# Kernel tuning notes

Measured on AMD Instinct MI355X. Metric: run time of the kernel, lower is better.

## Reference

```python
import jax, jax.numpy as jnp
import numpy as np

V, FN, CIN, HID, PTS = 50000, 100000, 3, 256, 10000
TEMP = 0.1
EPS = 1e-20


def line_mesh_graph(f, Vn):
    # f: [F,3] int triangles. Build the 'line mesh': one node per unique mesh edge.
    fe = jnp.concatenate([f[:, :2], f[:, 1:], f[:, jnp.array([2, 0])]], 0)  # [3F,2]
    fe = jnp.sort(fe, axis=1)
    keys = fe[:, 0] * Vn + fe[:, 1]                       # [3F] unique key per undirected edge
    ukeys, inv = jnp.unique(keys, return_inverse=True)
    edge_node = jnp.stack([ukeys // Vn, ukeys % Vn], -1)  # [E,2] endpoints of each edge-node
    E = ukeys.shape[0]
    feid = inv.reshape(3, -1).T                           # [F,3] edge-node id per face edge
    # line-graph connectivity: edges of the same face are mutual neighbors, plus self-loops
    srcs, dsts = [], []
    for i, j in ((0, 1), (1, 0), (1, 2), (2, 1), (2, 0), (0, 2)):
        srcs.append(feid[:, i]); dsts.append(feid[:, j])
    loop = jnp.arange(E)
    edge = jnp.stack([jnp.concatenate(srcs + [loop]), jnp.concatenate(dsts + [loop])], 0)  # [2,NE]
    return edge, edge_node, keys


def gsn_conv(x, edge, Ws, Wn, b):
    # GSNConv stand-in: self transform + mean-aggregated neighbor transform
    s, d = edge[0], edge[1]
    N = x.shape[0]
    deg = jax.ops.segment_sum(jnp.ones_like(s, x.dtype), d, num_segments=N)
    agg = jax.ops.segment_sum(x[s], d, num_segments=N) / jnp.clip(deg, 1.0)[:, None]
    return x @ Ws + agg @ Wn + b


def gumbel_mask(logits, temperature, num, key):
    U = jax.random.uniform(key, logits.shape)
    g = -jnp.log(-jnp.log(U + EPS) + EPS)
    y = jax.nn.softmax((logits + g) / temperature, -1)[:, 0]  # [E]
    _, ind = jax.lax.top_k(y, num)
    y_hard = jnp.zeros_like(y).at[ind].set(1.0)
    mask = jax.lax.stop_gradient(y_hard - y) + y              # straight-through one-hot
    return mask, y_hard == 1.0


def mesh_collapse(f, keys, pool_edge, Vn):
    # Vectorized replacement of the per-pool-edge python loop: hash-join pooled edge keys
    # against all 3F face-edge keys via sorted search.
    PE = pool_edge.shape[0]
    pool_idx = jnp.arange(Vn, Vn + PE)
    edge_keys = keys.reshape(3, -1).T                     # [F,3] (cols: e01,e12,e20)
    pk = pool_edge[:, 0] * Vn + pool_edge[:, 1]
    order = jnp.argsort(pk); pks = pk[order]
    flat = edge_keys.reshape(-1)
    pos = jnp.clip(jnp.searchsorted(pks, flat), 0, PE - 1)
    found = pks[pos] == flat
    pei = jnp.where(found, pool_idx[order[pos]], -1).reshape(-1, 3)  # pool_edge_idx [F,3]
    fm = found.reshape(-1, 3)
    pen = fm.sum(1)                                       # pool_edge_num per face
    psi = (fm * jnp.arange(3)).sum(1)                     # pool_start_idx per face
    vv = jnp.stack([f[:, 0], pei[:, 0], f[:, 1], pei[:, 1], f[:, 2], pei[:, 2]], -1)
    nf0 = f[pen == 0]
    fv1 = vv[pen == 1]; s1 = psi[pen == 1]
    fv1 = jnp.concatenate([fv1[s1 == 0], jnp.roll(fv1[s1 == 1], -2, 1), jnp.roll(fv1[s1 == 2], 2, 1)], 0)
    nf1 = jnp.concatenate([jnp.stack([fv1[:, 0], fv1[:, 1], fv1[:, 4]], -1),
                           jnp.stack([fv1[:, 1], fv1[:, 2], fv1[:, 4]], -1)], 0)
    fv2 = vv[pen == 2]; s2 = psi[pen == 2]
    fv2 = jnp.concatenate([fv2[s2 == 1], jnp.roll(fv2[s2 == 2], 2, 1), jnp.roll(fv2[s2 == 3], -2, 1)], 0)
    nf2 = jnp.concatenate([jnp.stack([fv2[:, 0], fv2[:, 1], fv2[:, 4]], -1),
                           jnp.stack([fv2[:, 1], fv2[:, 2], fv2[:, 3]], -1),
                           jnp.stack([fv2[:, 1], fv2[:, 3], fv2[:, 4]], -1)], 0)
    fv3 = vv[pen == 3]
    nf3 = jnp.concatenate([jnp.stack([fv3[:, 0], fv3[:, 1], fv3[:, 5]], -1),
                           jnp.stack([fv3[:, 1], fv3[:, 2], fv3[:, 3]], -1),
                           jnp.stack([fv3[:, 1], fv3[:, 3], fv3[:, 5]], -1),
                           jnp.stack([fv3[:, 3], fv3[:, 4], fv3[:, 5]], -1)], 0)
    new_faces = jnp.concatenate([nf0, nf1, nf2, nf3], 0)
    ne = jnp.concatenate([new_faces[:, :2], new_faces[:, 1:], new_faces[:, jnp.array([2, 0])]], 0)
    ai = jnp.arange(Vn + PE)
    ne = jnp.concatenate([jnp.stack([ai, ai], -1), ne], 0)
    return new_faces, ne.T


def setup_inputs():
    key = jax.random.key(0)
    ks = jax.random.split(key, 10)
    s1 = 1.0 / np.sqrt(CIN); s2 = 1.0 / np.sqrt(HID)
    return {
        'input': jax.random.normal(ks[0], (1, V, CIN), jnp.float32),
        'face': jax.random.randint(ks[1], (1, FN, 3), 0, V),
        'coord': jax.random.normal(ks[2], (1, V, 3), jnp.float32),
        'detail_points': jax.random.normal(ks[3], (1, PTS, 3), jnp.float32),
        'div': 5,
        'W1s': jax.random.normal(ks[4], (CIN, HID), jnp.float32) * s1,
        'W1n': jax.random.normal(ks[5], (CIN, HID), jnp.float32) * s1,
        'b1': jnp.zeros((HID,), jnp.float32),
        'W2s': jax.random.normal(ks[6], (HID, 2), jnp.float32) * s2,
        'W2n': jax.random.normal(ks[7], (HID, 2), jnp.float32) * s2,
        'b2': jnp.zeros((2,), jnp.float32),
    }


def reference(input, face, coord, detail_points, div, W1s, W1n, b1, W2s, W2n, b2):
    # B=1 (data-dependent per-sample output sizes make batch stacking only valid then)
    x0, f = input[0], face[0]
    Vn = x0.shape[0]
    edge, edge_node, keys = line_mesh_graph(f, Vn)
    xe = 0.5 * (x0[edge_node[:, 0]] + x0[edge_node[:, 1]])   # edge-node features [E,C]
    h = jax.nn.relu(gsn_conv(xe, edge, W1s, W1n, b1))
    out = jax.nn.sigmoid(gsn_conv(h, edge, W2s, W2n, b2))    # [E,2]
    mask, pool_ind = gumbel_mask(out, TEMP, out.shape[0] // div, jax.random.key(42))
    pool_edge = edge_node[pool_ind]                          # [PE,2]
    new_faces, new_edges = mesh_collapse(f, keys, pool_edge, Vn)
    return edge_node[None], new_faces[None], new_edges[None], mask[None]
```

## Files before the change

kernel.cpp:

```cpp
#include <hip/hip_runtime.h>
#include <stdint.h>

typedef uint32_t u32;
typedef uint64_t u64;

#define VN 50000
#define FN 100000
#define K3F 300000
#define EMAX 300000
#define NB1 1172
#define NBS 293
#define NBH 293
#define NBC 98
#define HALF1 150016
#define NBL 586

#define W_KPA    0u
#define W_KPB    600000u
#define W_SEGOFF 1200000u
#define W_FEID   1500004u
#define W_XE     1800004u
#define W_PK     2700004u
#define W_P      2703076u
#define W_Q      3303076u
#define W_Y      3903076u
#define W_YMAP   4203076u
#define W_T64    4503076u
#define W_SEL    5103140u
#define W_SELR   5403140u
#define W_CAT    5703140u
#define W_CATR   5803140u
#define W_NFI    5903140u
#define W_HIST   7103140u
#define W_HIST2  7403172u
#define W_SUMS   7703204u
#define W_CATH   7707300u
#define W_TKH    7708324u
#define W_DONE   7708580u
#define W_SCAL   7708612u

#define S_E 0
#define S_NUM 1
#define S_PFX 2
#define S_KREM 3
#define S_TU 4
#define S_R 5
#define S_NF 6
#define S_NEN 7
#define S_O1 8
#define S_O2 9
#define S_O3 10
#define S_RS 16
#define S_GS 24
#define S_GP 32

__device__ __forceinline__ void tf2x32(u32 x0, u32 x1, u32& o0, u32& o1) {
  const u32 ks0 = 0u, ks1 = 42u, ks2 = 0x1BD11BDAu ^ 0u ^ 42u;
  x0 += ks0; x1 += ks1;
#define TFR(r) { x0 += x1; x1 = (x1<<(r))|(x1>>(32-(r))); x1 ^= x0; }
  TFR(13) TFR(15) TFR(26) TFR(6)   x0 += ks1; x1 += ks2 + 1u;
  TFR(17) TFR(29) TFR(16) TFR(24)  x0 += ks2; x1 += ks0 + 2u;
  TFR(13) TFR(15) TFR(26) TFR(6)   x0 += ks0; x1 += ks1 + 3u;
  TFR(17) TFR(29) TFR(16) TFR(24)  x0 += ks1; x1 += ks2 + 4u;
  TFR(13) TFR(15) TFR(26) TFR(6)   x0 += ks2; x1 += ks0 + 5u;
#undef TFR
  o0 = x0; o1 = x1;
}

__global__ void scan_blocks(const u32* __restrict__ in, u32* __restrict__ out,
                            u32* __restrict__ sums, int n, u32* __restrict__ zeronext) {
  __shared__ u32 lds[256];
  int t = threadIdx.x;
  int base = blockIdx.x*1024 + t*4;
  u32 v[4]; u32 tot = 0;
  for (int k = 0; k < 4; ++k) { v[k] = (base+k < n) ? in[base+k] : 0u; tot += v[k]; }
  lds[t] = tot; __syncthreads();
  for (int o = 1; o < 256; o <<= 1) {
    u32 x = (t >= o) ? lds[t-o] : 0u; __syncthreads();
    lds[t] += x; __syncthreads();
  }
  u32 excl = lds[t] - tot;
  if (t == 255) sums[blockIdx.x] = lds[255];
  u32 run = excl;
  for (int k = 0; k < 4; ++k) {
    if (base+k < n) {
      out[base+k] = run;
      if (zeronext) zeronext[base+k] = 0u;
    }
    run += v[k];
  }
}

__global__ void scan_flagblocks(const u64* __restrict__ kp, u32* __restrict__ out,
                                u32* __restrict__ sums, int n) {
  __shared__ u32 lds[256];
  int t = threadIdx.x;
  int base = blockIdx.x*1024 + t*4;
  u32 v[4]; u32 tot = 0;
  for (int k = 0; k < 4; ++k) {
    int i = base + k;
    u32 f = 0;
    if (i < n) f = (i == 0 || (u32)(kp[i-1]>>32) != (u32)(kp[i]>>32)) ? 1u : 0u;
    v[k] = f; tot += f;
  }
  lds[t] = tot; __syncthreads();
  for (int o = 1; o < 256; o <<= 1) {
    u32 x = (t >= o) ? lds[t-o] : 0u; __syncthreads();
    lds[t] += x; __syncthreads();
  }
  u32 excl = lds[t] - tot;
  if (t == 255) sums[blockIdx.x] = lds[255];
  u32 run = excl;
  for (int k = 0; k < 4; ++k) { if (base+k < n) out[base+k] = run; run += v[k]; }
}

__global__ void scan_sums(u32* __restrict__ s, int nb) {
  __shared__ u32 lds[256];
  __shared__ u32 carry;
  int t = threadIdx.x;
  if (t == 0) carry = 0;
  __syncthreads();
  for (int base = 0; base < nb; base += 1024) {
    int idx = base + t*4;
    u32 v[4]; u32 tot = 0;
    for (int k = 0; k < 4; ++k) { v[k] = (idx+k < nb) ? s[idx+k] : 0u; tot += v[k]; }
    lds[t] = tot; __syncthreads();
    for (int o = 1; o < 256; o <<= 1) {
      u32 x = (t >= o) ? lds[t-o] : 0u; __syncthreads();
      lds[t] += x; __syncthreads();
    }
    u32 excl = lds[t] - tot;
    u32 ctot = lds[255];
    u32 c = carry;
    __syncthreads();
    u32 run = c + excl;
    for (int k = 0; k < 4; ++k) { if (idx+k < nb) s[idx+k] = run; run += v[k]; }
    if (t == 0) carry = c + ctot;
    __syncthreads();
  }
}

__global__ void scan64_src(const u32* __restrict__ ymap, const u32* __restrict__ scal,
                           u64* __restrict__ part, u64* __restrict__ sums) {
  __shared__ u64 lds[256];
  int t = threadIdx.x;
  int base = blockIdx.x*1024 + t*4;
  int E = (int)scal[S_E];
  u32 TU = scal[S_TU];
  u64 v[4]; u64 tot = 0;
  for (int k = 0; k < 4; ++k) {
    int e = base + k;
    u64 val = 0;
    if (e < E) {
      u32 u = ymap[e];
      if (u > TU) val = 1ull;
      else if (u == TU) val = 1ull << 32;
    }
    v[k] = val; tot += val;
  }
  lds[t] = tot; __syncthreads();
  for (int o = 1; o < 256; o <<= 1) {
    u64 x = (t >= o) ? lds[t-o] : 0ull; __syncthreads();
    lds[t] += x; __syncthreads();
  }
  u64 excl = lds[t] - tot;
  if (t == 255) sums[blockIdx.x] = lds[255];
  u64 run = excl;
  for (int k = 0; k < 4; ++k) { part[base+k] = run; run += v[k]; }
}

__global__ void scan64_sums(u64* __restrict__ s, int nb) {
  __shared__ u64 lds[256];
  int t = threadIdx.x;
  int idx = t*4;
  u64 v[4]; u64 tot = 0;
  for (int k = 0; k < 4; ++k) { v[k] = (idx+k < nb) ? s[idx+k] : 0ull; tot += v[k]; }
  lds[t] = tot; __syncthreads();
  for (int o = 1; o < 256; o <<= 1) {
    u64 x = (t >= o) ? lds[t-o] : 0ull; __syncthreads();
    lds[t] += x; __syncthreads();
  }
  u64 excl = lds[t] - tot;
  u64 run = excl;
  for (int k = 0; k < 4; ++k) { if (idx+k < nb) s[idx+k] = run; run += v[k]; }
}

__global__ void k_sel2(const u32* __restrict__ ymap, const u64* __restrict__ part,
                       const u64* __restrict__ sums, const u32* __restrict__ scal,
                       u32* __restrict__ sel, u32* __restrict__ selr) {
  int e = blockIdx.x*256 + threadIdx.x;
  if (e >= EMAX) return;
  int E = (int)scal[S_E];
  u32 TU = scal[S_TU], R = scal[S_R];
  u64 pre = part[e] + sums[e>>10];
  u32 GTpre = (u32)pre, TIEpre = (u32)(pre >> 32);
  u32 v = 0;
  if (e < E) {
    u32 u = ymap[e];
    v = (u > TU) || (u == TU && TIEpre < R);
  }
  sel[e] = v ? 1u : 0u;
  selr[e] = GTpre + min(TIEpre, R);
}

__global__ void k_rscat(const u64* __restrict__ kp, u64* __restrict__ okp,
                        const u32* __restrict__ hist, const u32* __restrict__ sums,
                        int shift, int nb, u32* __restrict__ histnext) {
  __shared__ u64 ball[4][8];
  __shared__ u64 vmask[4];
  int t = threadIdx.x, w = t>>6, lane = t&63;
  int i = blockIdx.x*256 + t;
  bool valid = i < K3F;
  u64 v = valid ? kp[i] : 0ull;
  u32 d = ((u32)(v>>32) >> shift) & 255u;
  for (int bit = 0; bit < 8; ++bit) {
    u64 bm = __ballot(valid && ((d>>bit)&1u));
    if (lane == 0) ball[w][bit] = bm;
  }
  u64 vb = __ballot(valid ? 1 : 0);
  if (lane == 0) vmask[w] = vb;
  __syncthreads();
  if (valid) {
    u32 rank = 0;
    for (int ww = 0; ww < w; ++ww) {
      u64 m = vmask[ww];
      for (int bit = 0; bit < 8; ++bit) { u64 bb = ball[ww][bit]; m &= ((d>>bit)&1u) ? bb : ~bb; }
      rank += (u32)__popcll(m);
    }
    u64 m = vmask[w];
    for (int bit = 0; bit < 8; ++bit) { u64 bb = ball[w][bit]; m &= ((d>>bit)&1u) ? bb : ~bb; }
    rank += (u32)__popcll(m & ((1ull<<lane)-1ull));
    u32 h = d*(u32)nb + blockIdx.x;
    u32 pos = hist[h] + sums[h>>10] + rank;
    okp[pos] = v;
    if (histnext) {
      u32 d2 = ((u32)(v>>32) >> (shift+8)) & 255u;
      atomicAdd(&histnext[d2*(u32)nb + (pos>>8)], 1u);
    }
  }
}

__global__ void k_keys(const int* __restrict__ face,
                       const float* __restrict__ W1s, const float* __restrict__ W1n,
                       const float* __restrict__ b1,
                       const float* __restrict__ W2s, const float* __restrict__ W2n,
                       float* __restrict__ pk,
                       u64* __restrict__ kp, u32* __restrict__ hist,
                       u32* __restrict__ tkh, u32* __restrict__ done) {
  __shared__ u32 h[256];
  int t = threadIdx.x;
  h[t] = 0;
  __syncthreads();
  if (blockIdx.x == 0) {
    tkh[t] = 0u;
    if (t < 32) done[t] = 0u;
    float* p = pk + t*12;
    p[0] = W1s[t]; p[1] = W1s[256+t]; p[2] = W1s[512+t];
    p[3] = W1n[t]; p[4] = W1n[256+t]; p[5] = W1n[512+t];
    p[6] = b1[t];
    p[7] = W2s[2*t]; p[8] = W2s[2*t+1];
    p[9] = W2n[2*t]; p[10] = W2n[2*t+1];
    p[11] = 0.0f;
  }
  int i = blockIdx.x*256 + t;
  if (i < K3F) {
    int s = i / FN, f = i - s*FN;
    int v0 = face[f*3 + s];
    int v1 = face[f*3 + (s == 2 ? 0 : s+1)];
    int a = min(v0, v1), b = max(v0, v1);
    u32 key = ((u32)a * (u32)VN + (u32)b) ^ 0x80000000u;
    kp[i] = ((u64)key << 32) | (u32)i;
    atomicAdd(&h[key & 255u], 1u);
  }
  __syncthreads();
  hist[(u32)t*NB1 + blockIdx.x] = h[t];
}

__global__ void k_uwrite(const u64* __restrict__ kp, const u32* __restrict__ rankp,
                         const u32* __restrict__ sums, const float* __restrict__ x,
                         u32* __restrict__ segoff, u32* __restrict__ feid,
                         float* __restrict__ xe, float* __restrict__ dout,
                         u32* __restrict__ scal, const int* __restrict__ divp) {
  int p = blockIdx.x*256 + threadIdx.x;
  if (p >= K3F) return;
  u64 v = kp[p];
  u32 cur = (u32)(v >> 32);
  u32 fl = (p == 0 || (u32)(kp[p-1] >> 32) != cur) ? 1u : 0u;
  u32 rk = rankp[p] + sums[p>>10];
  if (fl) {
    u32 e = rk;
    segoff[e] = (u32)p;
    int k = (int)(cur ^ 0x80000000u);
    long long kk = (long long)k;
    long long qq = (kk - (kk < 0 ? (long long)(VN-1) : 0ll)) / VN;
    int q = (int)qq;
    int r = (int)(kk - qq * VN);
    dout[2*e]   = (float)q;
    dout[2*e+1] = (float)r;
    u32 i0 = (u32)(q < 0 ? q + VN : q);
    u32 i1 = (u32)r;
    for (int c = 0; c < 3; ++c) xe[e*3+c] = 0.5f*(x[i0*3+c] + x[i1*3+c]);
  }
  u32 id = rk - 1u + fl;
  u32 i = (u32)v;
  u32 s = i / FN, f = i - s*FN;
  feid[f*3 + s] = id;
  if (p == K3F-1) {
    u32 E = rk + fl;
    u32 num = E / (u32)divp[0];
    scal[S_E] = E; scal[S_NUM] = num;
    segoff[E] = (u32)K3F;
    scal[S_PFX] = 0u; scal[S_KREM] = num;
  }
}

__device__ __forceinline__ void agg_neighbors(int e, u32 st, u32 en,
                                              const u64* __restrict__ kp,
                                              const u32* __restrict__ feid,
                                              const float* __restrict__ v, int stride,
                                              float* acc0, float* acc1, float* acc2) {
  const int sslot[6] = {0,1,1,2,2,0};
  const int dslot[6] = {1,0,2,1,0,2};
  float c0 = 0.f, c1 = 0.f, c2 = 0.f;
  for (int b = 0; b < 6; ++b) {
    int j = dslot[b], isl = sslot[b];
    for (u32 p = st; p < en; ++p) {
      u32 i = (u32)kp[p];
      u32 s = i / FN;
      if ((int)s == j) {
        u32 f = i - s*FN;
        u32 u = feid[f*3 + isl];
        c0 += v[u*stride]; c1 += v[u*stride+1]; if (stride == 3) c2 += v[u*stride+2];
      }
    }
  }
  c0 += v[e*stride]; c1 += v[e*stride+1]; if (stride == 3) c2 += v[e*stride+2];
  *acc0 = c0; *acc1 = c1; *acc2 = c2;
}

__global__ void k_l12(const float* __restrict__ xe, const u32* __restrict__ segoff,
                      const u64* __restrict__ kp, const u32* __restrict__ feid,
                      const u32* __restrict__ scal, const float* __restrict__ pk,
                      float* __restrict__ P, float* __restrict__ Q) {
  int e1 = blockIdx.x*256 + threadIdx.x;
  int E = (int)scal[S_E];
  if (e1 >= E) return;
  int e2 = e1 + HALF1;
  bool v2 = e2 < E;
  int e2c = v2 ? e2 : e1;
  u32 st1 = segoff[e1], en1 = segoff[e1+1];
  u32 st2 = segoff[e2c], en2 = segoff[e2c+1];
  float c0a,c1a,c2a, c0b,c1b,c2b;
  agg_neighbors(e1,  st1, en1, kp, feid, xe, 3, &c0a,&c1a,&c2a);
  agg_neighbors(e2c, st2, en2, kp, feid, xe, 3, &c0b,&c1b,&c2b);
  float x0a=xe[e1*3],  x1a=xe[e1*3+1],  x2a=xe[e1*3+2];
  float x0b=xe[e2c*3], x1b=xe[e2c*3+1], x2b=xe[e2c*3+2];
  float dga = (float)(2u*(en1-st1)+1u), dgb = (float)(2u*(en2-st2)+1u);
  float m0a=c0a/dga, m1a=c1a/dga, m2a=c2a/dga;
  float m0b=c0b/dgb, m1b=c1b/dgb, m2b=c2b/dgb;
  float p0a=0,p1a=0,q0a=0,q1a=0, p0b=0,p1b=0,q0b=0,q1b=0;
#pragma unroll 4
  for (int hh = 0; hh < 256; ++hh) {
    const float* w = pk + hh*12;
    float w0=w[0],w1=w[1],w2=w[2],w3=w[3],w4=w[4],w5=w[5],w6=w[6];
    float w7=w[7],w8=w[8],w9=w[9],w10=w[10];
    float s1a = x0a*w0 + x1a*w1 + x2a*w2;
    float s2a = m0a*w3 + m1a*w4 + m2a*w5;
    float ha = fmaxf(s1a + s2a + w6, 0.0f);
    p0a += ha*w7;  p1a += ha*w8;  q0a += ha*w9;  q1a += ha*w10;
    float s1b = x0b*w0 + x1b*w1 + x2b*w2;
    float s2b = m0b*w3 + m1b*w4 + m2b*w5;
    float hb = fmaxf(s1b + s2b + w6, 0.0f);
    p0b += hb*w7;  p1b += hb*w8;  q0b += hb*w9;  q1b += hb*w10;
  }
  P[2*e1] = p0a; P[2*e1+1] = p1a; Q[2*e1] = q0a; Q[2*e1+1] = q1a;
  if (v2) { P[2*e2] = p0b; P[2*e2+1] = p1b; Q[2*e2] = q0b; Q[2*e2+1] = q1b; }
}

__device__ __forceinline__ void score_one(int e, const float* P, const float* Q,
                                          const u32* segoff, const u64* kp, const u32* feid,
                                          float b20, float b21, float* yo, u32* ymo) {
  u32 st = segoff[e], en = segoff[e+1];
  float a0, a1, dummy;
  agg_neighbors(e, st, en, kp, feid, Q, 2, &a0, &a1, &dummy);
  float dg = (float)(2u*(en - st) + 1u);
  float z0 = P[2*e]   + a0/dg + b20;
  float z1 = P[2*e+1] + a1/dg + b21;
  float l0 = 1.0f/(1.0f + expf(-z0));
  float l1 = 1.0f/(1.0f + expf(-z1));
  u32 g0b, g1b;
  { u32 o0,o1; tf2x32(0u, 2u*(u32)e,      o0, o1); g0b = o0 ^ o1; }
  { u32 o0,o1; tf2x32(0u, 2u*(u32)e + 1u, o0, o1); g1b = o0 ^ o1; }
  float U0 = __uint_as_float((g0b>>9) | 0x3f800000u) - 1.0f;
  float U1 = __uint_as_float((g1b>>9) | 0x3f800000u) - 1.0f;
  float g0 = -logf(-logf(U0 + 1e-20f) + 1e-20f);
  float g1 = -logf(-logf(U1 + 1e-20f) + 1e-20f);
  float A0 = (l0 + g0)/0.1f;
  float A1 = (l1 + g1)/0.1f;
  float mx = fmaxf(A0, A1);
  float e0 = expf(A0-mx), e1v = expf(A1-mx);
  float y = e0/(e0+e1v);
  *yo = y;
  *ymo = __float_as_uint(y) | 0x80000000u;
}

__global__ void k_scores(const float* __restrict__ P, const float* __restrict__ Q,
                         const u32* __restrict__ segoff, const u64* __restrict__ kp,
                         const u32* __restrict__ feid,
                         const float* __restrict__ b2, const u32* __restrict__ scal,
                         float* __restrict__ Y, u32* __restrict__ ymap) {
  int e1 = blockIdx.x*256 + threadIdx.x;
  int E = (int)scal[S_E];
  if (e1 >= E) return;
  int e2 = e1 + HALF1;
  bool v2 = e2 < E;
  int e2c = v2 ? e2 : e1;
  float b20 = b2[0], b21 = b2[1];
  float ya, yb; u32 ma, mb;
  score_one(e1,  P, Q, segoff, kp, feid, b20, b21, &ya, &ma);
  score_one(e2c, P, Q, segoff, kp, feid, b20, b21, &yb, &mb);
  Y[e1] = ya; ymap[e1] = ma;
  if (v2) { Y[e2] = yb; ymap[e2] = mb; }
}

__global__ void k_tkround(const u32* __restrict__ ymap, u32* __restrict__ scal,
                          u32* __restrict__ hist, u32* __restrict__ done, int byte) {
  __shared__ u32 h[256];
  __shared__ u32 s2[256];
  __shared__ u32 chosen_s;
  __shared__ u32 lastflag;
  int t = threadIdx.x;
  h[t] = 0u;
  if (t == 0) lastflag = 0u;
  __syncthreads();
  int E = (int)scal[S_E];
  u32 pfx = scal[S_PFX];
  int base = blockIdx.x*1024;
  for (int k = 0; k < 4; ++k) {
    int e = base + k*256 + t;
    if (e < E) {
      u32 u = ymap[e];
      bool match = (byte == 3) || ((u >> ((byte+1)*8)) == pfx);
      if (match) atomicAdd(&h[(u >> (byte*8)) & 255u], 1u);
    }
  }
  __syncthreads();
  u32 c = h[t];
  if (c) atomicAdd(&hist[t], c);
  __syncthreads();
  if (t == 0) {
    __threadfence();
    u32 old = atomicAdd(&done[byte], 1u);
    if (old == gridDim.x - 1u) lastflag = 1u;
  }
  __syncthreads();
  if (!lastflag) return;
  __threadfence();
  u32 v = atomicExch(&hist[t], 0u);
  s2[t] = v;
  if (t == 0) chosen_s = 0u;
  __syncthreads();
  for (int o = 1; o < 256; o <<= 1) {
    u32 x = (t + o < 256) ? s2[t+o] : 0u; __syncthreads();
    s2[t] += x; __syncthreads();
  }
  u32 krem = scal[S_KREM];
  if (s2[t] >= krem) atomicMax(&chosen_s, (u32)t);
  __syncthreads();
  if (t == 0) {
    u32 chosen = chosen_s;
    u32 sufnext = (chosen < 255u) ? s2[chosen+1] : 0u;
    u32 newkrem = krem - sufnext;
    u32 npfx = (scal[S_PFX] << 8) | chosen;
    scal[S_PFX] = npfx; scal[S_KREM] = newkrem;
    if (byte == 0) { scal[S_TU] = npfx; scal[S_R] = newkrem; }
  }
}

__global__ void k_catfused(const u32* __restrict__ feid, const u32* __restrict__ sel,
                           u32* __restrict__ cat, u32* __restrict__ ch) {
  __shared__ u32 h[8];
  int t = threadIdx.x;
  if (t < 8) h[t] = 0u;
  __syncthreads();
  int base = blockIdx.x*1024 + t*4;
  for (int k = 0; k < 4; ++k) {
    int f = base + k;
    if (f < FN) {
      u32 m0 = sel[feid[f*3]], m1 = sel[feid[f*3+1]], m2 = sel[feid[f*3+2]];
      u32 pen = m0 + m1 + m2;
      u32 psi = m1 + 2u*m2;
      u32 c = (pen == 0) ? 0u : (pen == 1) ? (1u+psi) : (pen == 2) ? (3u+psi) : 7u;
      cat[f] = c;
      atomicAdd(&h[c], 1u);
    }
  }
  __syncthreads();
  if (t < 8) ch[(u32)t*NBC + blockIdx.x] = h[t];
}

__global__ void k_catoff(u32* __restrict__ ch, u32* __restrict__ scal) {
  __shared__ u32 lds[256];
  __shared__ u32 ex[1024];
  int t = threadIdx.x;
  u32 v[4]; u32 tot = 0;
  for (int k = 0; k < 4; ++k) {
    int i = t*4 + k;
    u32 x = (i < 8*NBC) ? ch[i] : 0u;
    v[k] = x; tot += x;
  }
  lds[t] = tot; __syncthreads();
  for (int o = 1; o < 256; o <<= 1) {
    u32 x = (t >= o) ? lds[t-o] : 0u; __syncthreads();
    lds[t] += x; __syncthreads();
  }
  u32 excl = lds[t] - tot;
  u32 run = excl;
  for (int k = 0; k < 4; ++k) { ex[t*4+k] = run; run += v[k]; }
  __syncthreads();
  for (int k = 0; k < 4; ++k) {
    int i = t*4 + k;
    if (i < 8*NBC) ch[i] = ex[i];
  }
  if (t == 0) {
    u32 total = lds[255];
    u32 bnd[9];
    for (int c = 0; c < 8; ++c) bnd[c] = ex[c*NBC];
    bnd[8] = total;
    u32 tot8[8];
    for (int c = 0; c < 8; ++c) tot8[c] = bnd[c+1] - bnd[c];
    u32 n0 = tot8[0], n1 = tot8[1]+tot8[2]+tot8[3], n2 = tot8[4]+tot8[5]+tot8[6], n3 = tot8[7];
    u32 NF = n0 + 2u*n1 + 3u*n2 + 4u*n3;
    u32 E = scal[S_E], num = scal[S_NUM];
    u32 NEn = (u32)VN + num + 3u*NF;
    scal[S_NF] = NF; scal[S_NEN] = NEn;
    scal[S_O1] = 2u*E;
    scal[S_O2] = 2u*E + 3u*NF;
    scal[S_O3] = 2u*E + 3u*NF + 2u*NEn;
    u32 RS[8] = {0u, n0,n0,n0, n0+2u*n1, n0+2u*n1, n0+2u*n1, n0+2u*n1+3u*n2};
    u32 GS[8] = {0u, n1,n1,n1, n2,n2,n2, n3};
    u32 GP[8] = {0u, n0,n0,n0, n0+n1, n0+n1, n0+n1, n0+n1+n2};
    for (int i = 0; i < 8; ++i) { scal[S_RS+i] = RS[i]; scal[S_GS+i] = GS[i]; scal[S_GP+i] = GP[i]; }
  }
}

__global__ void k_catrank(const u32* __restrict__ cat, const u32* __restrict__ ch,
                          u32* __restrict__ cr) {
  __shared__ u32 lds[256];
  int t = threadIdx.x;
  int base = blockIdx.x*1024 + t*4;
  u32 cc[4], loc[4];
  u32 cnt[8] = {0,0,0,0,0,0,0,0};
  for (int k = 0; k < 4; ++k) {
    int i = base + k;
    if (i < FN) { u32 c = cat[i]; cc[k] = c; loc[k] = cnt[c]++; }
    else cc[k] = 8u;
  }
  u32 tb[8];
  for (int c = 0; c < 8; ++c) {
    lds[t] = cnt[c]; __syncthreads();
    for (int o = 1; o < 256; o <<= 1) {
      u32 x = (t >= o) ? lds[t-o] : 0u; __syncthreads();
      lds[t] += x; __syncthreads();
    }
    tb[c] = lds[t] - cnt[c];
    __syncthreads();
  }
  for (int k = 0; k < 4; ++k) {
    int i = base + k;
    if (i < FN) { u32 c = cc[k]; cr[i] = ch[c*NBC + blockIdx.x] + tb[c] + loc[k]; }
  }
}

__global__ void k_wfaces(const int* __restrict__ face, const u32* __restrict__ cat,
                         const u32* __restrict__ cr, const u32* __restrict__ feid,
                         const u32* __restrict__ selr, const u32* __restrict__ scal,
                         int* __restrict__ nfi, float* __restrict__ dout) {
  int f = blockIdx.x*256 + threadIdx.x;
  if (f >= FN) return;
  const int nfc[8] = {1,2,2,2,3,3,3,4};
  const int tri[8][4][3] = {
    {{0,2,4},{0,0,0},{0,0,0},{0,0,0}},
    {{0,1,4},{1,2,4},{0,0,0},{0,0,0}},
    {{2,3,0},{3,4,0},{0,0,0},{0,0,0}},
    {{4,5,2},{5,0,2},{0,0,0},{0,0,0}},
    {{0,1,4},{1,2,3},{1,3,4},{0,0,0}},
    {{4,5,2},{5,0,1},{5,1,2},{0,0,0}},
    {{2,3,0},{3,4,5},{3,5,0},{0,0,0}},
    {{0,1,5},{1,2,3},{1,3,5},{3,4,5}}};
  u32 c = cat[f];
  int cv[6];
  cv[0] = face[f*3];   cv[2] = face[f*3+1]; cv[4] = face[f*3+2];
  cv[1] = VN + (int)selr[feid[f*3]];
  cv[3] = VN + (int)selr[feid[f*3+1]];
  cv[5] = VN + (int)selr[feid[f*3+2]];
  u32 g  = cr[f] - scal[S_GP + c];
  u32 o1 = scal[S_O1];
  for (int j = 0; j < nfc[c]; ++j) {
    u32 row = scal[S_RS + c] + (u32)j*scal[S_GS + c] + g;
    for (int m = 0; m < 3; ++m) {
      int v = cv[tri[c][j][m]];
      nfi[row*3 + m] = v;
      dout[o1 + row*3 + m] = (float)v;
    }
  }
}

__global__ void k_wne(const int* __restrict__ nfi, const u32* __restrict__ scal,
                      float* __restrict__ dout) {
  int i = blockIdx.x*256 + threadIdx.x;
  u32 NEn = scal[S_NEN];
  if (i >= (int)NEn) return;
  u32 NF = scal[S_NF];
  u32 Vp = (u32)VN + scal[S_NUM];
  u32 o2 = scal[S_O2];
  int a, b;
  if ((u32)i < Vp) { a = i; b = i; }
  else {
    u32 j = (u32)i - Vp;
    u32 blk = j / NF, r = j - blk*NF;
    int i0 = (blk == 0) ? 0 : (blk == 1) ? 1 : 2;
    int i1 = (blk == 0) ? 1 : (blk == 1) ? 2 : 0;
    a = nfi[r*3 + i0]; b = nfi[r*3 + i1];
  }
  dout[o2 + i] = (float)a;
  dout[o2 + NEn + i] = (float)b;
}

__global__ void k_wmask(const u32* __restrict__ sel, const float* __restrict__ Y,
                        const u32* __restrict__ scal, float* __restrict__ dout) {
  int e = blockIdx.x*256 + threadIdx.x;
  if (e >= (int)scal[S_E]) return;
  float y = Y[e];
  float yh = sel[e] ? 1.0f : 0.0f;
  dout[scal[S_O3] + e] = (yh - y) + y;
}

static void radix_pass(u32* hist, u32* histnext, u32* sums, u64* kin, u64* kout,
                       int shift, hipStream_t st) {
  scan_blocks<<<NBS, 256, 0, st>>>(hist, hist, sums, NB1*256, histnext);
  scan_sums<<<1, 256, 0, st>>>(sums, NBS);
  k_rscat<<<NB1, 256, 0, st>>>(kin, kout, hist, sums, shift, NB1, histnext);
}

extern "C" void kernel_launch(void* const* d_in, const int* in_sizes, int n_in,
                              void* d_out, int out_size, void* d_ws, size_t ws_size,
                              hipStream_t stream) {
  const float* x    = (const float*)d_in[0];
  const int*   face = (const int*)d_in[1];
  const int*   divp = (const int*)d_in[4];
  const float* W1s  = (const float*)d_in[5];
  const float* W1n  = (const float*)d_in[6];
  const float* b1   = (const float*)d_in[7];
  const float* W2s  = (const float*)d_in[8];
  const float* W2n  = (const float*)d_in[9];
  const float* b2   = (const float*)d_in[10];
  float* out = (float*)d_out;
  u32* W = (u32*)d_ws;

  u64 *KPA = (u64*)(W+W_KPA), *KPB = (u64*)(W+W_KPB);
  u32 *HIST = W+W_HIST, *HIST2 = W+W_HIST2, *SUMS = W+W_SUMS, *SCAL = W+W_SCAL;
  u32 *TKH = W+W_TKH, *DONE = W+W_DONE;
  u32 *RK = W+W_T64;
  u64 *T64 = (u64*)(W+W_T64);
  u64 *SUMS64 = (u64*)(W+W_SUMS);

  k_keys<<<NB1, 256, 0, stream>>>(face, W1s, W1n, b1, W2s, W2n, (float*)(W+W_PK),
                                  KPA, HIST, TKH, DONE);
  radix_pass(HIST,  HIST2,   SUMS, KPA, KPB,  0, stream);
  radix_pass(HIST2, HIST,    SUMS, KPB, KPA,  8, stream);
  radix_pass(HIST,  HIST2,   SUMS, KPA, KPB, 16, stream);
  radix_pass(HIST2, nullptr, SUMS, KPB, KPA, 24, stream);
  scan_flagblocks<<<NBS, 256, 0, stream>>>(KPA, RK, SUMS, K3F);
  scan_sums<<<1, 256, 0, stream>>>(SUMS, NBS);
  k_uwrite<<<NB1, 256, 0, stream>>>(KPA, RK, SUMS, x, W+W_SEGOFF, W+W_FEID,
                                    (float*)(W+W_XE), out, SCAL, divp);

  k_l12<<<NBL, 256, 0, stream>>>((float*)(W+W_XE), W+W_SEGOFF, KPA, W+W_FEID, SCAL,
                                 (float*)(W+W_PK), (float*)(W+W_P), (float*)(W+W_Q));
  k_scores<<<NBL, 256, 0, stream>>>((float*)(W+W_P), (float*)(W+W_Q), W+W_SEGOFF, KPA,
                                    W+W_FEID, b2, SCAL, (float*)(W+W_Y), W+W_YMAP);

  for (int byte = 3; byte >= 0; --byte)
    k_tkround<<<NBH, 256, 0, stream>>>(W+W_YMAP, SCAL, TKH, DONE, byte);
  scan64_src<<<NBS, 256, 0, stream>>>(W+W_YMAP, SCAL, T64, SUMS64);
  scan64_sums<<<1, 256, 0, stream>>>(SUMS64, NBS);
  k_sel2<<<NB1, 256, 0, stream>>>(W+W_YMAP, T64, SUMS64, SCAL, W+W_SEL, W+W_SELR);

  k_catfused<<<NBC, 256, 0, stream>>>(W+W_FEID, W+W_SEL, W+W_CAT, W+W_CATH);
  k_catoff<<<1, 256, 0, stream>>>(W+W_CATH, SCAL);
  k_catrank<<<NBC, 256, 0, stream>>>(W+W_CAT, W+W_CATH, W+W_CATR);
  k_wfaces<<<391, 256, 0, stream>>>(face, W+W_CAT, W+W_CATR, W+W_FEID, W+W_SELR, SCAL,
                                    (int*)(W+W_NFI), out);
  k_wne<<<5118, 256, 0, stream>>>((int*)(W+W_NFI), SCAL, out);
  k_wmask<<<NB1, 256, 0, stream>>>(W+W_SEL, (float*)(W+W_Y), SCAL, out);
}
```

Baseline: 343.7 us.

## Fold single-block sum scans into consumers and split next-pass histogram out of scatter

Removes the single-block scan_sums and scan64_sums launches. Each consumer (k_rscat, k_uwrite, k_sel2) now recomputes its block-prefix from the raw block sums in shared memory. The global atomic histogram for the next radix pass is dropped from the scatter and replaced by a separate k_rhist kernel that uses shared-memory atomics and writes per-block counts. k_sel2 is regrouped so each block handles 1024 elements. The aim is fewer serial single-block launches and fewer contended global atomics, paid for with redundant per-block prefix work and an extra read pass over the keys for each histogram.

```diff
diff --git a/kernel.cpp b/kernel.cpp
--- a/kernel.cpp
+++ b/kernel.cpp
@@ -68,7 +68,7 @@
 }
 
 __global__ void scan_blocks(const u32* __restrict__ in, u32* __restrict__ out,
-                            u32* __restrict__ sums, int n, u32* __restrict__ zeronext) {
+                            u32* __restrict__ sums, int n) {
   __shared__ u32 lds[256];
   int t = threadIdx.x;
   int base = blockIdx.x*1024 + t*4;
@@ -82,13 +82,7 @@
   u32 excl = lds[t] - tot;
   if (t == 255) sums[blockIdx.x] = lds[255];
   u32 run = excl;
-  for (int k = 0; k < 4; ++k) {
-    if (base+k < n) {
-      out[base+k] = run;
-      if (zeronext) zeronext[base+k] = 0u;
-    }
-    run += v[k];
-  }
+  for (int k = 0; k < 4; ++k) { if (base+k < n) out[base+k] = run; run += v[k]; }
 }
 
 __global__ void scan_flagblocks(const u64* __restrict__ kp, u32* __restrict__ out,
@@ -112,32 +106,6 @@
   if (t == 255) sums[blockIdx.x] = lds[255];
   u32 run = excl;
   for (int k = 0; k < 4; ++k) { if (base+k < n) out[base+k] = run; run += v[k]; }
-}
-
-__global__ void scan_sums(u32* __restrict__ s, int nb) {
-  __shared__ u32 lds[256];
-  __shared__ u32 carry;
-  int t = threadIdx.x;
-  if (t == 0) carry = 0;
-  __syncthreads();
-  for (int base = 0; base < nb; base += 1024) {
-    int idx = base + t*4;
-    u32 v[4]; u32 tot = 0;
-    for (int k = 0; k < 4; ++k) { v[k] = (idx+k < nb) ? s[idx+k] : 0u; tot += v[k]; }
-    lds[t] = tot; __syncthreads();
-    for (int o = 1; o < 256; o <<= 1) {
-      u32 x = (t >= o) ? lds[t-o] : 0u; __syncthreads();
-      lds[t] += x; __syncthreads();
-    }
-    u32 excl = lds[t] - tot;
-    u32 ctot = lds[255];
-    u32 c = carry;
-    __syncthreads();
-    u32 run = c + excl;
-    for (int k = 0; k < 4; ++k) { if (idx+k < nb) s[idx+k] = run; run += v[k]; }
-    if (t == 0) carry = c + ctot;
-    __syncthreads();
-  }
 }
 
 __global__ void scan64_src(const u32* __restrict__ ymap, const u32* __restrict__ scal,
@@ -169,46 +137,69 @@
   for (int k = 0; k < 4; ++k) { part[base+k] = run; run += v[k]; }
 }
 
-__global__ void scan64_sums(u64* __restrict__ s, int nb) {
-  __shared__ u64 lds[256];
-  int t = threadIdx.x;
-  int idx = t*4;
-  u64 v[4]; u64 tot = 0;
-  for (int k = 0; k < 4; ++k) { v[k] = (idx+k < nb) ? s[idx+k] : 0ull; tot += v[k]; }
-  lds[t] = tot; __syncthreads();
-  for (int o = 1; o < 256; o <<= 1) {
-    u64 x = (t >= o) ? lds[t-o] : 0ull; __syncthreads();
-    lds[t] += x; __syncthreads();
-  }
-  u64 excl = lds[t] - tot;
-  u64 run = excl;
-  for (int k = 0; k < 4; ++k) { if (idx+k < nb) s[idx+k] = run; run += v[k]; }
-}
-
 __global__ void k_sel2(const u32* __restrict__ ymap, const u64* __restrict__ part,
                        const u64* __restrict__ sums, const u32* __restrict__ scal,
                        u32* __restrict__ sel, u32* __restrict__ selr) {
-  int e = blockIdx.x*256 + threadIdx.x;
-  if (e >= EMAX) return;
+  __shared__ u64 sl64[256];
+  int t = threadIdx.x, b = blockIdx.x;
+  u64 partial = 0;
+  for (int j = t; j < b; j += 256) partial += sums[j];
+  sl64[t] = partial; __syncthreads();
+  for (int o = 128; o; o >>= 1) { if (t < o) sl64[t] += sl64[t+o]; __syncthreads(); }
+  u64 basepre = sl64[0];
   int E = (int)scal[S_E];
   u32 TU = scal[S_TU], R = scal[S_R];
-  u64 pre = part[e] + sums[e>>10];
-  u32 GTpre = (u32)pre, TIEpre = (u32)(pre >> 32);
-  u32 v = 0;
-  if (e < E) {
-    u32 u = ymap[e];
-    v = (u > TU) || (u == TU && TIEpre < R);
-  }
-  sel[e] = v ? 1u : 0u;
-  selr[e] = GTpre + min(TIEpre, R);
+  for (int k = 0; k < 4; ++k) {
+    int e = b*1024 + k*256 + t;
+    if (e >= EMAX) continue;
+    u64 pre = part[e] + basepre;
+    u32 GTpre = (u32)pre, TIEpre = (u32)(pre >> 32);
+    u32 v = 0;
+    if (e < E) {
+      u32 u = ymap[e];
+      v = (u > TU) || (u == TU && TIEpre < R);
+    }
+    sel[e] = v ? 1u : 0u;
+    selr[e] = GTpre + min(TIEpre, R);
+  }
+}
+
+__global__ void k_rhist(const u64* __restrict__ kp, u32* __restrict__ hist,
+                        int shift, int nb) {
+  __shared__ u32 h[256];
+  int t = threadIdx.x;
+  h[t] = 0; __syncthreads();
+  int i = blockIdx.x*256 + t;
+  if (i < K3F) atomicAdd(&h[((u32)(kp[i]>>32) >> shift) & 255u], 1u);
+  __syncthreads();
+  hist[(u32)t*nb + blockIdx.x] = h[t];
 }
 
 __global__ void k_rscat(const u64* __restrict__ kp, u64* __restrict__ okp,
                         const u32* __restrict__ hist, const u32* __restrict__ sums,
-                        int shift, int nb, u32* __restrict__ histnext) {
+                        int shift, int nb) {
+  __shared__ u32 sl[256];
+  __shared__ u32 ps[NBS];
   __shared__ u64 ball[4][8];
   __shared__ u64 vmask[4];
   int t = threadIdx.x, w = t>>6, lane = t&63;
+  u32 a0 = (t < NBS) ? sums[t] : 0u;
+  u32 a1 = (256 + t < NBS) ? sums[256+t] : 0u;
+  sl[t] = a0; __syncthreads();
+  for (int o = 1; o < 256; o <<= 1) {
+    u32 x = (t >= o) ? sl[t-o] : 0u; __syncthreads();
+    sl[t] += x; __syncthreads();
+  }
+  u32 incl0 = sl[t], tot0 = sl[255];
+  if (t < NBS) ps[t] = incl0 - a0;
+  __syncthreads();
+  sl[t] = a1; __syncthreads();
+  for (int o = 1; o < 256; o <<= 1) {
+    u32 x = (t >= o) ? sl[t-o] : 0u; __syncthreads();
+    sl[t] += x; __syncthreads();
+  }
+  if (256 + t < NBS) ps[256+t] = sl[t] - a1 + tot0;
+  __syncthreads();
   int i = blockIdx.x*256 + t;
   bool valid = i < K3F;
   u64 v = valid ? kp[i] : 0ull;
@@ -231,12 +222,8 @@
     for (int bit = 0; bit < 8; ++bit) { u64 bb = ball[w][bit]; m &= ((d>>bit)&1u) ? bb : ~bb; }
     rank += (u32)__popcll(m & ((1ull<<lane)-1ull));
     u32 h = d*(u32)nb + blockIdx.x;
-    u32 pos = hist[h] + sums[h>>10] + rank;
+    u32 pos = hist[h] + ps[h>>10] + rank;
     okp[pos] = v;
-    if (histnext) {
-      u32 d2 = ((u32)(v>>32) >> (shift+8)) & 255u;
-      atomicAdd(&histnext[d2*(u32)nb + (pos>>8)], 1u);
-    }
   }
 }
 
@@ -281,12 +268,20 @@
                          u32* __restrict__ segoff, u32* __restrict__ feid,
                          float* __restrict__ xe, float* __restrict__ dout,
                          u32* __restrict__ scal, const int* __restrict__ divp) {
-  int p = blockIdx.x*256 + threadIdx.x;
+  __shared__ u32 sl[256];
+  int t = threadIdx.x, b = blockIdx.x;
+  int chunk = b >> 2;
+  u32 partial = 0;
+  for (int j = t; j < chunk; j += 256) partial += sums[j];
+  sl[t] = partial; __syncthreads();
+  for (int o = 128; o; o >>= 1) { if (t < o) sl[t] += sl[t+o]; __syncthreads(); }
+  u32 basepre = sl[0];
+  int p = b*256 + t;
   if (p >= K3F) return;
   u64 v = kp[p];
   u32 cur = (u32)(v >> 32);
   u32 fl = (p == 0 || (u32)(kp[p-1] >> 32) != cur) ? 1u : 0u;
-  u32 rk = rankp[p] + sums[p>>10];
+  u32 rk = rankp[p] + basepre;
   if (fl) {
     u32 e = rk;
     segoff[e] = (u32)p;
@@ -636,13 +631,6 @@
   dout[scal[S_O3] + e] = (yh - y) + y;
 }
 
-static void radix_pass(u32* hist, u32* histnext, u32* sums, u64* kin, u64* kout,
-                       int shift, hipStream_t st) {
-  scan_blocks<<<NBS, 256, 0, st>>>(hist, hist, sums, NB1*256, histnext);
-  scan_sums<<<1, 256, 0, st>>>(sums, NBS);
-  k_rscat<<<NB1, 256, 0, st>>>(kin, kout, hist, sums, shift, NB1, histnext);
-}
-
 extern "C" void kernel_launch(void* const* d_in, const int* in_sizes, int n_in,
                               void* d_out, int out_size, void* d_ws, size_t ws_size,
                               hipStream_t stream) {
@@ -667,12 +655,19 @@
 
   k_keys<<<NB1, 256, 0, stream>>>(face, W1s, W1n, b1, W2s, W2n, (float*)(W+W_PK),
                                   KPA, HIST, TKH, DONE);
-  radix_pass(HIST,  HIST2,   SUMS, KPA, KPB,  0, stream);
-  radix_pass(HIST2, HIST,    SUMS, KPB, KPA,  8, stream);
-  radix_pass(HIST,  HIST2,   SUMS, KPA, KPB, 16, stream);
-  radix_pass(HIST2, nullptr, SUMS, KPB, KPA, 24, stream);
+  scan_blocks<<<NBS, 256, 0, stream>>>(HIST, HIST, SUMS, NB1*256);
+  k_rscat<<<NB1, 256, 0, stream>>>(KPA, KPB, HIST, SUMS,  0, NB1);
+  k_rhist<<<NB1, 256, 0, stream>>>(KPB, HIST2,  8, NB1);
+  scan_blocks<<<NBS, 256, 0, stream>>>(HIST2, HIST2, SUMS, NB1*256);
+  k_rscat<<<NB1, 256, 0, stream>>>(KPB, KPA, HIST2, SUMS,  8, NB1);
+  k_rhist<<<NB1, 256, 0, stream>>>(KPA, HIST, 16, NB1);
+  scan_blocks<<<NBS, 256, 0, stream>>>(HIST, HIST, SUMS, NB1*256);
+  k_rscat<<<NB1, 256, 0, stream>>>(KPA, KPB, HIST, SUMS, 16, NB1);
+  k_rhist<<<NB1, 256, 0, stream>>>(KPB, HIST2, 24, NB1);
+  scan_blocks<<<NBS, 256, 0, stream>>>(HIST2, HIST2, SUMS, NB1*256);
+  k_rscat<<<NB1, 256, 0, stream>>>(KPB, KPA, HIST2, SUMS, 24, NB1);
+
   scan_flagblocks<<<NBS, 256, 0, stream>>>(KPA, RK, SUMS, K3F);
-  scan_sums<<<1, 256, 0, stream>>>(SUMS, NBS);
   k_uwrite<<<NB1, 256, 0, stream>>>(KPA, RK, SUMS, x, W+W_SEGOFF, W+W_FEID,
                                     (float*)(W+W_XE), out, SCAL, divp);
 
@@ -684,8 +679,7 @@
   for (int byte = 3; byte >= 0; --byte)
     k_tkround<<<NBH, 256, 0, stream>>>(W+W_YMAP, SCAL, TKH, DONE, byte);
   scan64_src<<<NBS, 256, 0, stream>>>(W+W_YMAP, SCAL, T64, SUMS64);
-  scan64_sums<<<1, 256, 0, stream>>>(SUMS64, NBS);
-  k_sel2<<<NB1, 256, 0, stream>>>(W+W_YMAP, T64, SUMS64, SCAL, W+W_SEL, W+W_SELR);
+  k_sel2<<<NBS, 256, 0, stream>>>(W+W_YMAP, T64, SUMS64, SCAL, W+W_SEL, W+W_SELR);
 
   k_catfused<<<NBC, 256, 0, stream>>>(W+W_FEID, W+W_SEL, W+W_CAT, W+W_CATH);
   k_catoff<<<1, 256, 0, stream>>>(W+W_CATH, SCAL);
```

After: 316.3 us. -8.0%, faster.
